# Kernel tuning notes

Hardware: AMD Instinct MI355X
Metric: run time of the kernel (lower is better)

## Reference

```python
import jax, jax.numpy as jnp
import numpy as np

B, T, C, H = 64, 256, 384, 6
HS = C // H  # 64


def _ln(x, w, b, eps=1e-5):
    m = jnp.mean(x, axis=-1, keepdims=True)
    v = jnp.mean((x - m) ** 2, axis=-1, keepdims=True)
    return (x - m) / jnp.sqrt(v + eps) * w + b


def setup_inputs() -> dict:
    key = jax.random.key(0)
    ks = jax.random.split(key, 18)
    sc = 0.02
    return {
        "x": jax.random.normal(ks[0], (B, T, C), jnp.float32),
        "ln1_w": jnp.ones((C,), jnp.float32),
        "ln1_b": jnp.zeros((C,), jnp.float32),
        # per-head Q/K/V linears stacked over the head axis: [H, C, HS]
        "Wq": jax.random.normal(ks[1], (H, C, HS), jnp.float32) * sc,
        "bq": jnp.zeros((H, HS), jnp.float32),
        "Wk": jax.random.normal(ks[2], (H, C, HS), jnp.float32) * sc,
        "bk": jnp.zeros((H, HS), jnp.float32),
        "Wv": jax.random.normal(ks[3], (H, C, HS), jnp.float32) * sc,
        "bv": jnp.zeros((H, HS), jnp.float32),
        "Wproj": jax.random.normal(ks[4], (C, C), jnp.float32) * sc,
        "bproj": jnp.zeros((C,), jnp.float32),
        "ln2_w": jnp.ones((C,), jnp.float32),
        "ln2_b": jnp.zeros((C,), jnp.float32),
        "W1": jax.random.normal(ks[5], (C, 4 * C), jnp.float32) * sc,
        "b1": jnp.zeros((4 * C,), jnp.float32),
        "W2": jax.random.normal(ks[6], (4 * C, C), jnp.float32) * sc,
        "b2": jnp.zeros((C,), jnp.float32),
    }


def reference(x, ln1_w, ln1_b, Wq, bq, Wk, bk, Wv, bv, Wproj, bproj,
              ln2_w, ln2_b, W1, b1, W2, b2):
    # --- pre-norm causal MHA (dropout = identity in eval) ---
    h = _ln(x, ln1_w, ln1_b)
    Q = jnp.einsum('btc,hcd->bhtd', h, Wq) + bq[None, :, None, :]
    K = jnp.einsum('btc,hcd->bhtd', h, Wk) + bk[None, :, None, :]
    V = jnp.einsum('btc,hcd->bhtd', h, Wv) + bv[None, :, None, :]
    scores = jnp.einsum('bhtd,bhsd->bhts', Q, K) * (HS ** -0.5)
    mask = jnp.tril(jnp.ones((x.shape[1], x.shape[1]), bool))
    scores = jnp.where(mask, scores, -jnp.inf)
    wei = jax.nn.softmax(scores, axis=-1)
    o = jnp.einsum('bhts,bhsd->bhtd', wei, V)
    # concat heads (same order as torch.cat over head list)
    o = o.transpose(0, 2, 1, 3).reshape(x.shape[0], x.shape[1], C)
    x1 = x + o @ Wproj + bproj
    # --- pre-norm FFN with exact (erf) GELU, matching torch default ---
    h2 = _ln(x1, ln2_w, ln2_b)
    f = jax.nn.gelu(h2 @ W1 + b1, approximate=False) @ W2 + b2
    return x1 + f
```

## Files before the change

### kernel.cpp

```cpp
#include <hip/hip_runtime.h>
#include <math.h>

constexpr int Bsz  = 64;
constexpr int Tseq = 256;
constexpr int Cdim = 384;
constexpr int Hh   = 6;
constexpr int HSd  = 64;
constexpr int Mrows = Bsz * Tseq;
constexpr int Cffn  = 4 * Cdim;
constexpr int Nqkv  = 3 * Cdim;

typedef __attribute__((ext_vector_type(8))) short short8;
typedef __attribute__((ext_vector_type(4))) float f32x4;

__device__ __forceinline__ ushort f2bf(float x) {
  union { float f; uint u; } a; a.f = x;
  uint r = a.u + 0x7fffu + ((a.u >> 16) & 1u);
  return (ushort)(r >> 16);
}

__device__ __forceinline__ float gelu_fast(float x) {
  float t = x * x;
  float u = x * fmaf(0.044715f, t, 1.0f);
  float e = fminf(1.5957691216f * u, 80.f);
  float z = __expf(e);
  return x * (z / (1.0f + z));
}

__global__ __launch_bounds__(256) void prep_kernel(
    const float* __restrict__ Wq, const float* __restrict__ Wk,
    const float* __restrict__ Wv, const float* __restrict__ Wproj,
    const float* __restrict__ W1, const float* __restrict__ W2,
    const float* __restrict__ bq, const float* __restrict__ bk,
    const float* __restrict__ bv,
    ushort* __restrict__ WqkvT, ushort* __restrict__ WprojT,
    ushort* __restrict__ W1T, ushort* __restrict__ W2T,
    float* __restrict__ bqkv) {
  const int bid = blockIdx.x;
  if (bid >= 1728) {
    int i = (bid - 1728) * 256 + threadIdx.x;
    if (i < Nqkv)
      bqkv[i] = (i < 384) ? bq[i] : (i < 768) ? bk[i - 384] : bv[i - 768];
    return;
  }
  const int tx = threadIdx.x & 31, ty = threadIdx.x >> 5;
  const float* src; ushort* dst; int R, S, r0, s0;
  if (bid < 432) {
    int which = bid / 144, rem = bid % 144;
    const float* W = (which == 0) ? Wq : (which == 1) ? Wk : Wv;
    int bz = rem / 24, t = rem % 24;
    R = 384; S = 64;
    src = W + (size_t)bz * R * S;
    dst = WqkvT + (size_t)which * 384 * 384 + (size_t)bz * R * S;
    r0 = (t >> 1) * 32; s0 = (t & 1) * 32;
  } else if (bid < 576) {
    int rem = bid - 432; R = 384; S = 384; src = Wproj; dst = WprojT;
    r0 = (rem / 12) * 32; s0 = (rem % 12) * 32;
  } else if (bid < 1152) {
    int rem = bid - 576; R = 384; S = 1536; src = W1; dst = W1T;
    r0 = (rem / 48) * 32; s0 = (rem % 48) * 32;
  } else {
    int rem = bid - 1152; R = 1536; S = 384; src = W2; dst = W2T;
    r0 = (rem / 12) * 32; s0 = (rem % 12) * 32;
  }
  __shared__ float t[32][33];
#pragma unroll
  for (int i = 0; i < 32; i += 8)
    t[ty + i][tx] = src[(size_t)(r0 + ty + i) * S + s0 + tx];
  __syncthreads();
#pragma unroll
  for (int i = 0; i < 32; i += 8)
    dst[(size_t)(s0 + ty + i) * R + r0 + tx] = f2bf(t[tx][ty + i]);
}

__global__ __launch_bounds__(256) void ln_kernel(
    const float* __restrict__ x, const float* __restrict__ w,
    const float* __restrict__ b, ushort* __restrict__ out, int nrows) {
  int row  = blockIdx.x * 4 + (threadIdx.x >> 6);
  int lane = threadIdx.x & 63;
  if (row >= nrows) return;
  const float* xr = x + (size_t)row * Cdim;
  float v[6];
  float s = 0.f;
#pragma unroll
  for (int i = 0; i < 6; ++i) { v[i] = xr[lane + 64 * i]; s += v[i]; }
#pragma unroll
  for (int off = 32; off > 0; off >>= 1) s += __shfl_xor(s, off, 64);
  float mean = s * (1.f / Cdim);
  float sq = 0.f;
#pragma unroll
  for (int i = 0; i < 6; ++i) { float d = v[i] - mean; sq += d * d; }
#pragma unroll
  for (int off = 32; off > 0; off >>= 1) sq += __shfl_xor(sq, off, 64);
  float rstd = rsqrtf(sq * (1.f / Cdim) + 1e-5f);
  ushort* orow = out + (size_t)row * Cdim;
#pragma unroll
  for (int i = 0; i < 6; ++i) {
    int c = lane + 64 * i;
    orow[c] = f2bf((v[i] - mean) * rstd * w[c] + b[c]);
  }
}

template <int EPI, int BN>
__global__ __launch_bounds__(256) void mfma_gemm(
    const ushort* __restrict__ A, const ushort* __restrict__ Bt,
    const float* __restrict__ bias, const float* __restrict__ res,
    void* __restrict__ Cout, void* __restrict__ C2, void* __restrict__ C3,
    int M, int N, int K) {
  constexpr int WC = BN / 2;
  constexpr int JN = WC / 16;
  __shared__ ushort Als[128 * 32];
  __shared__ ushort Bls[BN * 32];
  const int tid = threadIdx.x;

  const int lid = blockIdx.y * gridDim.x + blockIdx.x;
  const int xcd = lid & 7, idx = lid >> 3;
  const int by = xcd * 16 + (idx & 15);
  const int bx = idx >> 4;
  const int m0 = by * 128, n0 = bx * BN;

  const int lane = tid & 63;
  const int w    = tid >> 6;
  const int wr   = (w >> 1) * 64;
  const int wc   = (w & 1) * WC;
  const int lm   = lane & 15;
  const int g    = lane >> 4;
  const int rq   = g * 4;

  const int c0 = tid, c1 = tid + 256;
  const int wbase = (tid & ~63) * 8;
  const int kcs = (((c0 & 3) ^ ((c0 >> 3) & 3)) * 8);
  const int kqs = (g ^ ((lm >> 1) & 3)) * 8;

  f32x4 acc[4][JN] = {};

  for (int k0 = 0; k0 < K; k0 += 32) {
    const ushort* gA0 = A  + (size_t)(m0 + (c0 >> 2)) * K + k0 + kcs;
    const ushort* gA1 = A  + (size_t)(m0 + (c1 >> 2)) * K + k0 + kcs;
    const ushort* gB0 = Bt + (size_t)(n0 + (c0 >> 2)) * K + k0 + kcs;
    __syncthreads();
    __builtin_amdgcn_global_load_lds(
        (const __attribute__((address_space(1))) uint*)gA0,
        (__attribute__((address_space(3))) uint*)(Als + wbase), 16, 0, 0);
    __builtin_amdgcn_global_load_lds(
        (const __attribute__((address_space(1))) uint*)gA1,
        (__attribute__((address_space(3))) uint*)(Als + wbase + 2048), 16, 0, 0);
    __builtin_amdgcn_global_load_lds(
        (const __attribute__((address_space(1))) uint*)gB0,
        (__attribute__((address_space(3))) uint*)(Bls + wbase), 16, 0, 0);
    if constexpr (BN == 128) {
      const ushort* gB1 = Bt + (size_t)(n0 + (c1 >> 2)) * K + k0 + kcs;
      __builtin_amdgcn_global_load_lds(
          (const __attribute__((address_space(1))) uint*)gB1,
          (__attribute__((address_space(3))) uint*)(Bls + wbase + 2048), 16, 0, 0);
    }
    __syncthreads();

    short8 af[4], bf[JN];
#pragma unroll
    for (int i = 0; i < 4; ++i)
      af[i] = *(const short8*)&Als[(wr + i * 16 + lm) * 32 + kqs];
#pragma unroll
    for (int j = 0; j < JN; ++j)
      bf[j] = *(const short8*)&Bls[(wc + j * 16 + lm) * 32 + kqs];
#pragma unroll
    for (int i = 0; i < 4; ++i)
#pragma unroll
      for (int j = 0; j < JN; ++j)
        acc[i][j] = __builtin_amdgcn_mfma_f32_16x16x32_bf16(af[i], bf[j],
                                                            acc[i][j], 0, 0, 0);
  }

  float bb[JN];
#pragma unroll
  for (int j = 0; j < JN; ++j) bb[j] = bias[n0 + wc + j * 16 + lm];

#pragma unroll
  for (int i = 0; i < 4; ++i) {
#pragma unroll
    for (int r = 0; r < 4; ++r) {
      const int row = m0 + wr + i * 16 + rq + r;
      if (EPI == 1) {
        const float* resrow = res + (size_t)row * N + n0 + wc;
        float* crow = (float*)Cout + (size_t)row * N + n0 + wc;
#pragma unroll
        for (int j = 0; j < JN; ++j) {
          float rv = __builtin_nontemporal_load(resrow + j * 16 + lm);
          crow[j * 16 + lm] = acc[i][j][r] + bb[j] + rv;
        }
      } else if (EPI == 3) {
        const int bb_ = row >> 8, tt = row & 255;
#pragma unroll
        for (int j = 0; j < JN; ++j) {
          const int colb = n0 + wc + j * 16;
          const int sec = colb / 384, cc = colb % 384;
          const int hh = cc >> 6, db = (cc & 63) + lm;
          ushort* dstp = (sec == 0) ? (ushort*)Cout
                       : (sec == 1) ? (ushort*)C2 : (ushort*)C3;
          dstp[((size_t)(bb_ * Hh + hh) * Tseq + tt) * HSd + db] =
              f2bf(acc[i][j][r] + bb[j]);
        }
      } else {
        ushort* crow = (ushort*)Cout + (size_t)row * N + n0 + wc;
#pragma unroll
        for (int j = 0; j < JN; ++j) {
          float v = acc[i][j][r] + bb[j];
          if (EPI == 2) v = gelu_fast(v);
          crow[j * 16 + lm] = f2bf(v);
        }
      }
    }
  }
}

__global__ __launch_bounds__(256) void attn_kernel(
    const ushort* __restrict__ Qb, const ushort* __restrict__ Kb,
    const ushort* __restrict__ Vb, ushort* __restrict__ Oc) {
  __shared__ ushort Ks[64 * 72];
  __shared__ ushort Vt[64 * 72];
  __shared__ ushort Pl[4][16 * 72];
  const int bh = blockIdx.x, qt = blockIdx.y;
  const int b = bh / Hh, h = bh % Hh;
  const int tid = threadIdx.x;
  const int w = tid >> 6, lane = tid & 63;
  const int g = lane >> 4, n16 = lane & 15;

  const ushort* qrow = Qb + ((size_t)bh * Tseq + qt * 64 + w * 16 + n16) * HSd;
  short8 qf0 = *(const short8*)(qrow + g * 8);
  short8 qf1 = *(const short8*)(qrow + 32 + g * 8);

  f32x4 oacc[4] = {};
  float m_r[4], l_r[4];
#pragma unroll
  for (int r = 0; r < 4; ++r) { m_r[r] = -1e30f; l_r[r] = 0.f; }

  const int t0 = qt * 64 + w * 16 + g * 4;

  const ushort* Ksrc = Kb + (size_t)bh * Tseq * HSd;
  const ushort* Vsrc = Vb + (size_t)bh * Tseq * HSd;

  for (int st = 0; st <= qt; ++st) {
    __syncthreads();
    for (int c = tid; c < 512; c += 256) {
      int kr = c >> 3, kc = (c & 7) * 8;
      *(uint4*)&Ks[kr * 72 + kc] =
          *(const uint4*)&Ksrc[(size_t)(st * 64 + kr) * HSd + kc];
      int vr = c & 63, vc = (c >> 6) * 8;
      uint4 vv = *(const uint4*)&Vsrc[(size_t)(st * 64 + vr) * HSd + vc];
      const ushort* pv = (const ushort*)&vv;
#pragma unroll
      for (int i = 0; i < 8; ++i) Vt[(vc + i) * 72 + vr] = pv[i];
    }
    __syncthreads();

    f32x4 s[4];
#pragma unroll
    for (int ct = 0; ct < 4; ++ct) {
      short8 kf0 = *(const short8*)&Ks[(ct * 16 + n16) * 72 + g * 8];
      short8 kf1 = *(const short8*)&Ks[(ct * 16 + n16) * 72 + 32 + g * 8];
      f32x4 z = {};
      z = __builtin_amdgcn_mfma_f32_16x16x32_bf16(qf0, kf0, z, 0, 0, 0);
      z = __builtin_amdgcn_mfma_f32_16x16x32_bf16(qf1, kf1, z, 0, 0, 0);
      s[ct] = z;
    }

#pragma unroll
    for (int ct = 0; ct < 4; ++ct) {
      const int s_col = st * 64 + ct * 16 + n16;
#pragma unroll
      for (int r = 0; r < 4; ++r) {
        float v = s[ct][r] * 0.125f;
        s[ct][r] = (s_col > t0 + r) ? -1e30f : v;
      }
    }

#pragma unroll
    for (int r = 0; r < 4; ++r) {
      float m = fmaxf(fmaxf(s[0][r], s[1][r]), fmaxf(s[2][r], s[3][r]));
      m = fmaxf(m, __shfl_xor(m, 1, 64));
      m = fmaxf(m, __shfl_xor(m, 2, 64));
      m = fmaxf(m, __shfl_xor(m, 4, 64));
      m = fmaxf(m, __shfl_xor(m, 8, 64));
      float mnew = fmaxf(m_r[r], m);
      float alpha = __expf(m_r[r] - mnew);
      m_r[r] = mnew;
      float ssum = 0.f;
#pragma unroll
      for (int ct = 0; ct < 4; ++ct) {
        float p = __expf(s[ct][r] - mnew);
        s[ct][r] = p;
        ssum += p;
      }
      ssum += __shfl_xor(ssum, 1, 64);
      ssum += __shfl_xor(ssum, 2, 64);
      ssum += __shfl_xor(ssum, 4, 64);
      ssum += __shfl_xor(ssum, 8, 64);
      l_r[r] = l_r[r] * alpha + ssum;
#pragma unroll
      for (int j = 0; j < 4; ++j) oacc[j][r] *= alpha;
    }

    ushort* pw = &Pl[w][0];
#pragma unroll
    for (int ct = 0; ct < 4; ++ct)
#pragma unroll
      for (int r = 0; r < 4; ++r)
        pw[(g * 4 + r) * 72 + ct * 16 + n16] = f2bf(s[ct][r]);

    short8 pf0 = *(const short8*)&pw[n16 * 72 + g * 8];
    short8 pf1 = *(const short8*)&pw[n16 * 72 + 32 + g * 8];
#pragma unroll
    for (int j = 0; j < 4; ++j) {
      short8 vf0 = *(const short8*)&Vt[(j * 16 + n16) * 72 + g * 8];
      short8 vf1 = *(const short8*)&Vt[(j * 16 + n16) * 72 + 32 + g * 8];
      oacc[j] = __builtin_amdgcn_mfma_f32_16x16x32_bf16(pf0, vf0, oacc[j], 0, 0, 0);
      oacc[j] = __builtin_amdgcn_mfma_f32_16x16x32_bf16(pf1, vf1, oacc[j], 0, 0, 0);
    }
  }

  float inv[4];
#pragma unroll
  for (int r = 0; r < 4; ++r) inv[r] = 1.f / l_r[r];
  ushort* orow = Oc + ((size_t)(b * Tseq + qt * 64 + w * 16)) * Cdim + h * HSd;
#pragma unroll
  for (int j = 0; j < 4; ++j)
#pragma unroll
    for (int r = 0; r < 4; ++r)
      orow[(size_t)(g * 4 + r) * Cdim + j * 16 + n16] = f2bf(oacc[j][r] * inv[r]);
}

extern "C" void kernel_launch(void* const* d_in, const int* in_sizes, int n_in,
                              void* d_out, int out_size, void* d_ws, size_t ws_size,
                              hipStream_t stream) {
  const float* x      = (const float*)d_in[0];
  const float* ln1_w  = (const float*)d_in[1];
  const float* ln1_b  = (const float*)d_in[2];
  const float* Wq     = (const float*)d_in[3];
  const float* bq     = (const float*)d_in[4];
  const float* Wk     = (const float*)d_in[5];
  const float* bk     = (const float*)d_in[6];
  const float* Wv     = (const float*)d_in[7];
  const float* bv     = (const float*)d_in[8];
  const float* Wproj  = (const float*)d_in[9];
  const float* bproj  = (const float*)d_in[10];
  const float* ln2_w  = (const float*)d_in[11];
  const float* ln2_b  = (const float*)d_in[12];
  const float* W1     = (const float*)d_in[13];
  const float* b1     = (const float*)d_in[14];
  const float* W2     = (const float*)d_in[15];
  const float* b2     = (const float*)d_in[16];
  float* out = (float*)d_out;

  char* p = (char*)d_ws;
  ushort* h     = (ushort*)p;  p += (size_t)Mrows * Cdim * 2;
  ushort* Qb    = (ushort*)p;
  float*  x1    = (float*)p;   p += (size_t)Mrows * HSd * Hh * 2;
  ushort* Kb    = (ushort*)p;  p += (size_t)Mrows * HSd * Hh * 2;
  ushort* Vb    = (ushort*)p;  p += (size_t)Mrows * HSd * Hh * 2;
  ushort* Oc    = (ushort*)p;  p += (size_t)Mrows * Cdim * 2;
  ushort* g     = (ushort*)p;  p += (size_t)Mrows * Cffn * 2;
  ushort* WqkvT = (ushort*)p;  p += (size_t)Nqkv * Cdim * 2;
  ushort* WprojT= (ushort*)p;  p += (size_t)Cdim * Cdim * 2;
  ushort* W1T   = (ushort*)p;  p += (size_t)Cffn * Cdim * 2;
  ushort* W2T   = (ushort*)p;  p += (size_t)Cdim * Cffn * 2;
  float*  bqkv  = (float*)p;   p += (size_t)Nqkv * 4;
  ushort* h2 = h;

  dim3 blk(256);

  prep_kernel<<<dim3(1733), blk, 0, stream>>>(Wq, Wk, Wv, Wproj, W1, W2,
                                              bq, bk, bv,
                                              WqkvT, WprojT, W1T, W2T, bqkv);

  ln_kernel<<<dim3(Mrows / 4), blk, 0, stream>>>(x, ln1_w, ln1_b, h, Mrows);

  mfma_gemm<3, 128><<<dim3(Nqkv / 128, Mrows / 128), blk, 0, stream>>>(
      h, WqkvT, bqkv, nullptr, Qb, Kb, Vb, Mrows, Nqkv, Cdim);

  attn_kernel<<<dim3(Bsz * Hh, 4), blk, 0, stream>>>(Qb, Kb, Vb, Oc);

  mfma_gemm<1, 64><<<dim3(Cdim / 64, Mrows / 128), blk, 0, stream>>>(
      Oc, WprojT, bproj, x, x1, nullptr, nullptr, Mrows, Cdim, Cdim);

  ln_kernel<<<dim3(Mrows / 4), blk, 0, stream>>>(x1, ln2_w, ln2_b, h2, Mrows);

  mfma_gemm<2, 128><<<dim3(Cffn / 128, Mrows / 128), blk, 0, stream>>>(
      h2, W1T, b1, nullptr, g, nullptr, nullptr, Mrows, Cffn, Cdim);

  mfma_gemm<1, 64><<<dim3(Cdim / 64, Mrows / 128), blk, 0, stream>>>(
      g, W2T, b2, x1, out, nullptr, nullptr, Mrows, Cdim, Cffn);
}
```

Baseline: 262.7 us.

## Double GEMM K-tile to 64 and store residual x1 in bf16

The GEMM K step per iteration doubles from 32 to 64, using a new 8-way XOR-swizzled LDS layout. This halves the number of barrier pairs per output tile and issues more MFMAs between syncs. Separately, the post-attention residual x1 is now stored as bf16 instead of fp32, and LN2 and the final GEMM epilogue read it as bf16. That cuts memory traffic but loses residual precision, which could affect accuracy against the fp32 reference.

```diff
diff --git a/kernel.cpp b/kernel.cpp
--- a/kernel.cpp
+++ b/kernel.cpp
@@ -17,6 +17,10 @@
   union { float f; uint u; } a; a.f = x;
   uint r = a.u + 0x7fffu + ((a.u >> 16) & 1u);
   return (ushort)(r >> 16);
+}
+__device__ __forceinline__ float bf2f(ushort u) {
+  union { uint u; float f; } a; a.u = ((uint)u) << 16;
+  return a.f;
 }
 
 __device__ __forceinline__ float gelu_fast(float x) {
@@ -73,17 +77,22 @@
     dst[(size_t)(s0 + ty + i) * R + r0 + tx] = f2bf(t[tx][ty + i]);
 }
 
+template <typename T>
 __global__ __launch_bounds__(256) void ln_kernel(
-    const float* __restrict__ x, const float* __restrict__ w,
+    const T* __restrict__ x, const float* __restrict__ w,
     const float* __restrict__ b, ushort* __restrict__ out, int nrows) {
   int row  = blockIdx.x * 4 + (threadIdx.x >> 6);
   int lane = threadIdx.x & 63;
   if (row >= nrows) return;
-  const float* xr = x + (size_t)row * Cdim;
+  const T* xr = x + (size_t)row * Cdim;
   float v[6];
   float s = 0.f;
 #pragma unroll
-  for (int i = 0; i < 6; ++i) { v[i] = xr[lane + 64 * i]; s += v[i]; }
+  for (int i = 0; i < 6; ++i) {
+    if constexpr (sizeof(T) == 2) v[i] = bf2f(xr[lane + 64 * i]);
+    else                          v[i] = xr[lane + 64 * i];
+    s += v[i];
+  }
 #pragma unroll
   for (int off = 32; off > 0; off >>= 1) s += __shfl_xor(s, off, 64);
   float mean = s * (1.f / Cdim);
@@ -104,13 +113,14 @@
 template <int EPI, int BN>
 __global__ __launch_bounds__(256) void mfma_gemm(
     const ushort* __restrict__ A, const ushort* __restrict__ Bt,
-    const float* __restrict__ bias, const float* __restrict__ res,
+    const float* __restrict__ bias, const void* __restrict__ res,
     void* __restrict__ Cout, void* __restrict__ C2, void* __restrict__ C3,
     int M, int N, int K) {
   constexpr int WC = BN / 2;
   constexpr int JN = WC / 16;
-  __shared__ ushort Als[128 * 32];
-  __shared__ ushort Bls[BN * 32];
+  constexpr int NB = BN / 32;
+  __shared__ ushort Als[128 * 64];
+  __shared__ ushort Bls[BN * 64];
   const int tid = threadIdx.x;
 
   const int lid = blockIdx.y * gridDim.x + blockIdx.x;
@@ -127,48 +137,53 @@
   const int g    = lane >> 4;
   const int rq   = g * 4;
 
-  const int c0 = tid, c1 = tid + 256;
-  const int wbase = (tid & ~63) * 8;
-  const int kcs = (((c0 & 3) ^ ((c0 >> 3) & 3)) * 8);
-  const int kqs = (g ^ ((lm >> 1) & 3)) * 8;
+  const int wub = (tid & ~63) * 8;
 
   f32x4 acc[4][JN] = {};
 
-  for (int k0 = 0; k0 < K; k0 += 32) {
-    const ushort* gA0 = A  + (size_t)(m0 + (c0 >> 2)) * K + k0 + kcs;
-    const ushort* gA1 = A  + (size_t)(m0 + (c1 >> 2)) * K + k0 + kcs;
-    const ushort* gB0 = Bt + (size_t)(n0 + (c0 >> 2)) * K + k0 + kcs;
+  for (int k0 = 0; k0 < K; k0 += 64) {
     __syncthreads();
-    __builtin_amdgcn_global_load_lds(
-        (const __attribute__((address_space(1))) uint*)gA0,
-        (__attribute__((address_space(3))) uint*)(Als + wbase), 16, 0, 0);
-    __builtin_amdgcn_global_load_lds(
-        (const __attribute__((address_space(1))) uint*)gA1,
-        (__attribute__((address_space(3))) uint*)(Als + wbase + 2048), 16, 0, 0);
-    __builtin_amdgcn_global_load_lds(
-        (const __attribute__((address_space(1))) uint*)gB0,
-        (__attribute__((address_space(3))) uint*)(Bls + wbase), 16, 0, 0);
-    if constexpr (BN == 128) {
-      const ushort* gB1 = Bt + (size_t)(n0 + (c1 >> 2)) * K + k0 + kcs;
+#pragma unroll
+    for (int q = 0; q < 4; ++q) {
+      const int ci = tid + q * 256;
+      const int row = ci >> 3;
+      const int kc = ((ci & 7) ^ (row & 7)) * 8;
+      const ushort* gA = A + (size_t)(m0 + row) * K + k0 + kc;
       __builtin_amdgcn_global_load_lds(
-          (const __attribute__((address_space(1))) uint*)gB1,
-          (__attribute__((address_space(3))) uint*)(Bls + wbase + 2048), 16, 0, 0);
+          (const __attribute__((address_space(1))) uint*)gA,
+          (__attribute__((address_space(3))) uint*)(Als + wub + q * 2048),
+          16, 0, 0);
+    }
+#pragma unroll
+    for (int q = 0; q < NB; ++q) {
+      const int ci = tid + q * 256;
+      const int row = ci >> 3;
+      const int kc = ((ci & 7) ^ (row & 7)) * 8;
+      const ushort* gB = Bt + (size_t)(n0 + row) * K + k0 + kc;
+      __builtin_amdgcn_global_load_lds(
+          (const __attribute__((address_space(1))) uint*)gB,
+          (__attribute__((address_space(3))) uint*)(Bls + wub + q * 2048),
+          16, 0, 0);
     }
     __syncthreads();
 
-    short8 af[4], bf[JN];
-#pragma unroll
-    for (int i = 0; i < 4; ++i)
-      af[i] = *(const short8*)&Als[(wr + i * 16 + lm) * 32 + kqs];
-#pragma unroll
-    for (int j = 0; j < JN; ++j)
-      bf[j] = *(const short8*)&Bls[(wc + j * 16 + lm) * 32 + kqs];
-#pragma unroll
-    for (int i = 0; i < 4; ++i)
+#pragma unroll
+    for (int half = 0; half < 2; ++half) {
+      const int sl = ((half << 2) | g) ^ (lm & 7);
+      short8 af[4], bf[JN];
+#pragma unroll
+      for (int i = 0; i < 4; ++i)
+        af[i] = *(const short8*)&Als[(wr + i * 16 + lm) * 64 + sl * 8];
 #pragma unroll
       for (int j = 0; j < JN; ++j)
-        acc[i][j] = __builtin_amdgcn_mfma_f32_16x16x32_bf16(af[i], bf[j],
-                                                            acc[i][j], 0, 0, 0);
+        bf[j] = *(const short8*)&Bls[(wc + j * 16 + lm) * 64 + sl * 8];
+#pragma unroll
+      for (int i = 0; i < 4; ++i)
+#pragma unroll
+        for (int j = 0; j < JN; ++j)
+          acc[i][j] = __builtin_amdgcn_mfma_f32_16x16x32_bf16(af[i], bf[j],
+                                                              acc[i][j], 0, 0, 0);
+    }
   }
 
   float bb[JN];
@@ -181,13 +196,19 @@
     for (int r = 0; r < 4; ++r) {
       const int row = m0 + wr + i * 16 + rq + r;
       if (EPI == 1) {
-        const float* resrow = res + (size_t)row * N + n0 + wc;
-        float* crow = (float*)Cout + (size_t)row * N + n0 + wc;
+        const float* resrow = (const float*)res + (size_t)row * N + n0 + wc;
+        ushort* crow = (ushort*)Cout + (size_t)row * N + n0 + wc;
 #pragma unroll
         for (int j = 0; j < JN; ++j) {
           float rv = __builtin_nontemporal_load(resrow + j * 16 + lm);
-          crow[j * 16 + lm] = acc[i][j][r] + bb[j] + rv;
+          crow[j * 16 + lm] = f2bf(acc[i][j][r] + bb[j] + rv);
         }
+      } else if (EPI == 4) {
+        const ushort* resrow = (const ushort*)res + (size_t)row * N + n0 + wc;
+        float* crow = (float*)Cout + (size_t)row * N + n0 + wc;
+#pragma unroll
+        for (int j = 0; j < JN; ++j)
+          crow[j * 16 + lm] = acc[i][j][r] + bb[j] + bf2f(resrow[j * 16 + lm]);
       } else if (EPI == 3) {
         const int bb_ = row >> 8, tt = row & 255;
 #pragma unroll
@@ -203,11 +224,8 @@
       } else {
         ushort* crow = (ushort*)Cout + (size_t)row * N + n0 + wc;
 #pragma unroll
-        for (int j = 0; j < JN; ++j) {
-          float v = acc[i][j][r] + bb[j];
-          if (EPI == 2) v = gelu_fast(v);
-          crow[j * 16 + lm] = f2bf(v);
-        }
+        for (int j = 0; j < JN; ++j)
+          crow[j * 16 + lm] = f2bf(gelu_fast(acc[i][j][r] + bb[j]));
       }
     }
   }
@@ -353,10 +371,9 @@
 
   char* p = (char*)d_ws;
   ushort* h     = (ushort*)p;  p += (size_t)Mrows * Cdim * 2;
-  ushort* Qb    = (ushort*)p;
-  float*  x1    = (float*)p;   p += (size_t)Mrows * HSd * Hh * 2;
-  ushort* Kb    = (ushort*)p;  p += (size_t)Mrows * HSd * Hh * 2;
-  ushort* Vb    = (ushort*)p;  p += (size_t)Mrows * HSd * Hh * 2;
+  ushort* Qb    = (ushort*)p;  p += (size_t)Mrows * Cdim * 2;
+  ushort* Kb    = (ushort*)p;  p += (size_t)Mrows * Cdim * 2;
+  ushort* Vb    = (ushort*)p;  p += (size_t)Mrows * Cdim * 2;
   ushort* Oc    = (ushort*)p;  p += (size_t)Mrows * Cdim * 2;
   ushort* g     = (ushort*)p;  p += (size_t)Mrows * Cffn * 2;
   ushort* WqkvT = (ushort*)p;  p += (size_t)Nqkv * Cdim * 2;
@@ -365,6 +382,7 @@
   ushort* W2T   = (ushort*)p;  p += (size_t)Cdim * Cffn * 2;
   float*  bqkv  = (float*)p;   p += (size_t)Nqkv * 4;
   ushort* h2 = h;
+  ushort* x1 = Qb;
 
   dim3 blk(256);
 
@@ -372,7 +390,7 @@
                                               bq, bk, bv,
                                               WqkvT, WprojT, W1T, W2T, bqkv);
 
-  ln_kernel<<<dim3(Mrows / 4), blk, 0, stream>>>(x, ln1_w, ln1_b, h, Mrows);
+  ln_kernel<float><<<dim3(Mrows / 4), blk, 0, stream>>>(x, ln1_w, ln1_b, h, Mrows);
 
   mfma_gemm<3, 128><<<dim3(Nqkv / 128, Mrows / 128), blk, 0, stream>>>(
       h, WqkvT, bqkv, nullptr, Qb, Kb, Vb, Mrows, Nqkv, Cdim);
@@ -382,11 +400,11 @@
   mfma_gemm<1, 64><<<dim3(Cdim / 64, Mrows / 128), blk, 0, stream>>>(
       Oc, WprojT, bproj, x, x1, nullptr, nullptr, Mrows, Cdim, Cdim);
 
-  ln_kernel<<<dim3(Mrows / 4), blk, 0, stream>>>(x1, ln2_w, ln2_b, h2, Mrows);
+  ln_kernel<ushort><<<dim3(Mrows / 4), blk, 0, stream>>>(x1, ln2_w, ln2_b, h2, Mrows);
 
   mfma_gemm<2, 128><<<dim3(Cffn / 128, Mrows / 128), blk, 0, stream>>>(
       h2, W1T, b1, nullptr, g, nullptr, nullptr, Mrows, Cffn, Cdim);
 
-  mfma_gemm<1, 64><<<dim3(Cdim / 64, Mrows / 128), blk, 0, stream>>>(
+  mfma_gemm<4, 64><<<dim3(Cdim / 64, Mrows / 128), blk, 0, stream>>>(
       g, W2T, b2, x1, out, nullptr, nullptr, Mrows, Cdim, Cffn);
 }
```

Result: faster. 253.0 us (-3.7%).
